# Kernel tuning notes

Hardware: AMD Instinct MI355X
Metric: run time of the kernel (lower is better)

## Reference

```python
import jax, jax.numpy as jnp
import numpy as np

EPS = 1e-8
K = 8  # group_size

def _l2norm(x):
    # matches torch F.normalize(p=2, eps): x / max(||x||, eps)
    n = jnp.linalg.norm(x, axis=-1, keepdims=True)
    return x / jnp.maximum(n, EPS)

def setup_inputs() -> dict:
    key = jax.random.key(0)
    k1, k2, k3, k4 = jax.random.split(key, 4)
    B, L, d = 8, 16384, 256
    max_groups = L // K
    token_vectors = jax.random.normal(k1, (B, L, d), dtype=jnp.float32)
    local_positions = jax.random.normal(k2, (K, d), dtype=jnp.float32)
    macro_positions = jax.random.normal(k3, (max_groups, d), dtype=jnp.float32)
    # learned params
    init_decay = 0.9
    decay_logit = jnp.full((d,), np.log(init_decay / (1.0 - init_decay)), dtype=jnp.float32)
    W_q = jax.random.normal(k4, (d, d), dtype=jnp.float32) * (1.0 / np.sqrt(d))
    return {"token_vectors": token_vectors, "local_positions": local_positions,
            "macro_positions": macro_positions, "decay_logit": decay_logit, "W_q": W_q}

def reference(token_vectors, local_positions, macro_positions, decay_logit, W_q):
    B, L, d = token_vectors.shape
    n_groups = L // K  # L chosen divisible by K; no remainder branch

    # ---- compute_groups: bind with local positions, mean over window, normalize
    full = token_vectors.reshape(B, n_groups, K, d)
    bound = full * local_positions[None, None]          # bind: elementwise product
    group_vecs = _l2norm(bound.mean(axis=2))            # [B, n_groups, d]

    # ---- causal EMA scan over groups with per-step L2 normalize
    alpha = jax.nn.sigmoid(decay_logit)                 # [d]
    def step(S, inp):
        g, mp = inp                                     # g: [B,d], mp: [d]
        S = _l2norm(alpha * S + (1.0 - alpha) * (g * mp))
        return S, S
    S0 = jnp.zeros((B, d), dtype=token_vectors.dtype)
    _, states = jax.lax.scan(step, S0, (group_vecs.transpose(1, 0, 2), macro_positions[:n_groups]))
    global_states = states.transpose(1, 0, 2)           # [B, n_groups, d]

    # ---- per-token queries from the state of the *previous* group
    t = jnp.arange(L)
    group_idx = t // K
    prev = jnp.maximum(group_idx - 1, 0)
    state = global_states[:, prev, :]                   # [B, L, d]
    state = jnp.where((group_idx < 1)[None, :, None], 0.0, state)
    local_pos = local_positions[t % K]                  # [L, d]
    queries = jnp.einsum('bld,ed->ble', state * local_pos[None], W_q)  # Linear: x @ W.T

    final_state = global_states[:, -1]
    return queries, final_state
```

## Files before the change

kernel.cpp:

```cpp
#include <hip/hip_runtime.h>
#include <hip/hip_bf16.h>

#define EPSV 1e-8f

typedef __attribute__((ext_vector_type(4))) float f32x4;
typedef __attribute__((ext_vector_type(8))) __bf16 bf16x8;
typedef __attribute__((ext_vector_type(8))) unsigned short ushort8;

static __device__ __forceinline__ unsigned short f2bf(float x) {
    __hip_bfloat16 h = __float2bfloat16(x);
    return *reinterpret_cast<unsigned short*>(&h);
}
static __device__ __forceinline__ float bf2f(unsigned short u) {
    __hip_bfloat16 h = *reinterpret_cast<__hip_bfloat16*>(&u);
    return __bfloat162float(h);
}

template <int CTRL, int RMASK = 0xf>
static __device__ __forceinline__ float dpp_add(float x) {
    int y = __builtin_amdgcn_update_dpp(0, __builtin_bit_cast(int, x), CTRL, RMASK, 0xf, true);
    return x + __builtin_bit_cast(float, y);
}

static __device__ __forceinline__ float wave_allsum(float x) {
    x = dpp_add<0xB1>(x);
    x = dpp_add<0x4E>(x);
    x = dpp_add<0x141>(x);
    x = dpp_add<0x140>(x);
    x = dpp_add<0x142, 0xa>(x);
    x = dpp_add<0x143, 0xc>(x);
    int t = __builtin_amdgcn_readlane(__builtin_bit_cast(int, x), 63);
    return __builtin_bit_cast(float, t);
}

__global__ __launch_bounds__(256) void build_bpt_kernel(const float* __restrict__ wq,
                                                        unsigned short* __restrict__ bpt) {
    int idx = blockIdx.x * 256 + threadIdx.x;
    int e = idx / 768;
    int j = idx - e * 768;
    int d = j & 255;
    int band = j >> 8;
    float w = wq[e * 256 + d];
    unsigned short hi = f2bf(w);
    unsigned short v;
    if (band == 1) v = f2bf(w - bf2f(hi));
    else           v = hi;
    bpt[idx] = v;
}

__global__ __launch_bounds__(256) void groupvec_kernel(const float* __restrict__ tv,
                                                       const float* __restrict__ lp,
                                                       const float* __restrict__ mp,
                                                       const float* __restrict__ dl,
                                                       float* __restrict__ v) {
    int bid = blockIdx.x;
    int g = bid & 2047;
    int d = threadIdx.x;
    const float* base = tv + (size_t)bid * 2048 + d;
    float acc = 0.f;
#pragma unroll
    for (int k = 0; k < 8; ++k)
        acc += base[k * 256] * lp[k * 256 + d];
    float m = acc * 0.125f;

    float p = m * m;
#pragma unroll
    for (int s = 1; s < 64; s <<= 1) p += __shfl_xor(p, s);
    __shared__ float red[4];
    if ((threadIdx.x & 63) == 0) red[threadIdx.x >> 6] = p;
    __syncthreads();
    float tot = red[0] + red[1] + red[2] + red[3];
    float n = sqrtf(tot);
    float inv = 1.0f / fmaxf(n, EPSV);

    float alpha = 1.0f / (1.0f + expf(-dl[d]));
    v[(size_t)bid * 256 + d] = (1.0f - alpha) * (m * inv) * mp[g * 256 + d];
}

__global__ __launch_bounds__(64) void scan_kernel(const float* __restrict__ v,
                                                  const float* __restrict__ dl,
                                                  float* __restrict__ states,
                                                  float* __restrict__ out) {
    int b = blockIdx.x;
    int lane = threadIdx.x;
    const float* vb = v + (size_t)b * 2048 * 256 + 4 * lane;
    float* sb = states + (size_t)b * 2048 * 256 + 4 * lane;

    f32x4 alpha;
#pragma unroll
    for (int i = 0; i < 4; ++i)
        alpha[i] = 1.0f / (1.0f + expf(-dl[4 * lane + i]));

    f32x4 buf[16];
#pragma unroll
    for (int j = 0; j < 16; ++j)
        buf[j] = *(const f32x4*)(vb + (size_t)j * 256);

    f32x4 w = {0.f, 0.f, 0.f, 0.f};
    float inv = 0.f;
    f32x4 S = {0.f, 0.f, 0.f, 0.f};

    for (int t = 0; t < 2048; t += 16) {
#pragma unroll
        for (int j = 0; j < 16; ++j) {
            const int g = t + j;
            f32x4 vcur = buf[j];
            const int gp = g + 16;
            if (gp < 2048) buf[j] = *(const f32x4*)(vb + (size_t)gp * 256);

            f32x4 u;
#pragma unroll
            for (int i = 0; i < 4; ++i) u[i] = fmaf(inv, w[i], vcur[i]);

            float m01 = fmaf(u[1], u[1], u[0] * u[0]);
            float m23 = fmaf(u[3], u[3], u[2] * u[2]);
            float ss = wave_allsum(m01 + m23);

            float ssc = fmaxf(ss, 1e-16f);
            float y0 = __builtin_amdgcn_rsqf(ssc);
            float h = 0.5f * ssc;
            float nr = fmaf(-h * y0, y0, 1.5f);
            inv = y0 * nr;

#pragma unroll
            for (int i = 0; i < 4; ++i) w[i] = alpha[i] * u[i];
#pragma unroll
            for (int i = 0; i < 4; ++i) S[i] = u[i] * inv;
            *(f32x4*)(sb + (size_t)g * 256) = S;
        }
    }
    *(f32x4*)(out + 33554432 + b * 256 + 4 * lane) = S;
}

__global__ __launch_bounds__(512) void queries_gemm_kernel(const float* __restrict__ states,
                                                           const float* __restrict__ lp,
                                                           const unsigned short* __restrict__ bpt,
                                                           float* __restrict__ out) {
    __shared__ unsigned short As[128 * 40];
    __shared__ unsigned short Bs[256 * 40];

    int tid = threadIdx.x;
    int lane = tid & 63;
    int wid = tid >> 6;
    int wm = wid >> 2;
    int wn = wid & 3;
    int row0 = blockIdx.x * 128;

    f32x4 acc[4][4];
#pragma unroll
    for (int i = 0; i < 4; ++i)
#pragma unroll
        for (int j = 0; j < 4; ++j) acc[i][j] = (f32x4){0.f, 0.f, 0.f, 0.f};

    int ar = tid >> 2;
    int aj0 = (tid & 3) * 8;
    int R = row0 + ar;
    int ab = R >> 14;
    int al = R & 16383;
    int ag = al >> 3;
    int ak = al & 7;
    const float* srow = (ag > 0) ? (states + ((size_t)(ab * 2048 + ag - 1)) * 256) : nullptr;
    const float* lrow = lp + ak * 256;

    int be = tid >> 1;
    int bj0 = (tid & 1) * 16;

    for (int c = 0; c < 24; ++c) {
        int kc = c * 32;
        int band = c >> 3;
        int dc = (c & 7) * 32;

        {
            float vals[8];
            if (ag == 0) {
#pragma unroll
                for (int i = 0; i < 8; ++i) vals[i] = 0.f;
            } else {
                f32x4 s0 = *(const f32x4*)(srow + dc + aj0);
                f32x4 s1 = *(const f32x4*)(srow + dc + aj0 + 4);
                f32x4 l0 = *(const f32x4*)(lrow + dc + aj0);
                f32x4 l1 = *(const f32x4*)(lrow + dc + aj0 + 4);
#pragma unroll
                for (int i = 0; i < 4; ++i) { vals[i] = s0[i] * l0[i]; vals[4 + i] = s1[i] * l1[i]; }
            }
            ushort8 h;
#pragma unroll
            for (int i = 0; i < 8; ++i) {
                unsigned short hi = f2bf(vals[i]);
                h[i] = (band < 2) ? hi : f2bf(vals[i] - bf2f(hi));
            }
            *(ushort8*)&As[ar * 40 + aj0] = h;
        }
        {
            const unsigned short* src = bpt + (size_t)be * 768 + kc + bj0;
            ushort8 b0 = *(const ushort8*)src;
            ushort8 b1 = *(const ushort8*)(src + 8);
            *(ushort8*)&Bs[be * 40 + bj0] = b0;
            *(ushort8*)&Bs[be * 40 + bj0 + 8] = b1;
        }
        __syncthreads();

        int lr = lane & 15;
        int lk = (lane >> 4) * 8;
        bf16x8 af[4], bfr[4];
#pragma unroll
        for (int mi = 0; mi < 4; ++mi) {
            ushort8 r = *(const ushort8*)&As[(wm * 64 + mi * 16 + lr) * 40 + lk];
            af[mi] = __builtin_bit_cast(bf16x8, r);
        }
#pragma unroll
        for (int ni = 0; ni < 4; ++ni) {
            ushort8 r = *(const ushort8*)&Bs[(wn * 64 + ni * 16 + lr) * 40 + lk];
            bfr[ni] = __builtin_bit_cast(bf16x8, r);
        }
#pragma unroll
        for (int mi = 0; mi < 4; ++mi)
#pragma unroll
            for (int ni = 0; ni < 4; ++ni)
                acc[mi][ni] = __builtin_amdgcn_mfma_f32_16x16x32_bf16(af[mi], bfr[ni], acc[mi][ni], 0, 0, 0);
        __syncthreads();
    }

    int cr = (lane >> 4) * 4;
    int cc = lane & 15;
#pragma unroll
    for (int mi = 0; mi < 4; ++mi) {
#pragma unroll
        for (int ni = 0; ni < 4; ++ni) {
            int Rg = row0 + wm * 64 + mi * 16 + cr;
            int E = wn * 64 + ni * 16 + cc;
#pragma unroll
            for (int q = 0; q < 4; ++q)
                out[(size_t)(Rg + q) * 256 + E] = acc[mi][ni][q];
        }
    }
}

extern "C" void kernel_launch(void* const* d_in, const int* in_sizes, int n_in,
                              void* d_out, int out_size, void* d_ws, size_t ws_size,
                              hipStream_t stream) {
    const float* tv = (const float*)d_in[0];
    const float* lp = (const float*)d_in[1];
    const float* mp = (const float*)d_in[2];
    const float* dl = (const float*)d_in[3];
    const float* wq = (const float*)d_in[4];
    float* out = (float*)d_out;

    float* v = (float*)d_ws;
    float* states = v + 4194304;
    unsigned short* bpt = (unsigned short*)(states + 4194304);

    build_bpt_kernel<<<768, 256, 0, stream>>>(wq, bpt);
    groupvec_kernel<<<16384, 256, 0, stream>>>(tv, lp, mp, dl, v);
    scan_kernel<<<8, 64, 0, stream>>>(v, dl, states, out);
    queries_gemm_kernel<<<1024, 512, 0, stream>>>(states, lp, bpt, out);
}
```

Measured before the change: 556.4 us.

## Break scan norm dependency and fold local positions into a per-group GEMM

The scan no longer waits on the norm of the current state before normalizing. It predicts the next squared norm algebraically from precomputed ||v||^2, the ||alpha*u||^2 term and the dot with the next input, so both wave reductions come off the critical recurrence. The local-position multiply moves into an expanded weight matrix (8x256 output columns per group), and the GEMM now works on per-group rows with precomputed bf16 hi/lo splits from a new convert kernel. This cuts A-side work in the GEMM. The cost is an extra kernel, a larger B matrix, and possible numerical drift from the expanded-norm formula.

Result: slower. 662.4 us (+19.1%).

```diff
diff --git a/kernel.cpp b/kernel.cpp
--- a/kernel.cpp
+++ b/kernel.cpp
@@ -4,6 +4,7 @@
 #define EPSV 1e-8f
 
 typedef __attribute__((ext_vector_type(4))) float f32x4;
+typedef __attribute__((ext_vector_type(4))) unsigned short u16x4;
 typedef __attribute__((ext_vector_type(8))) __bf16 bf16x8;
 typedef __attribute__((ext_vector_type(8))) unsigned short ushort8;
 
@@ -33,14 +34,17 @@
     return __builtin_bit_cast(float, t);
 }
 
-__global__ __launch_bounds__(256) void build_bpt_kernel(const float* __restrict__ wq,
+__global__ __launch_bounds__(256) void build_bpt_kernel(const float* __restrict__ lp,
+                                                        const float* __restrict__ wq,
                                                         unsigned short* __restrict__ bpt) {
     int idx = blockIdx.x * 256 + threadIdx.x;
-    int e = idx / 768;
-    int j = idx - e * 768;
+    int n = idx / 768;
+    int j = idx - n * 768;
     int d = j & 255;
     int band = j >> 8;
-    float w = wq[e * 256 + d];
+    int k = n >> 8;
+    int e = n & 255;
+    float w = lp[k * 256 + d] * wq[e * 256 + d];
     unsigned short hi = f2bf(w);
     unsigned short v;
     if (band == 1) v = f2bf(w - bf2f(hi));
@@ -52,7 +56,8 @@
                                                        const float* __restrict__ lp,
                                                        const float* __restrict__ mp,
                                                        const float* __restrict__ dl,
-                                                       float* __restrict__ v) {
+                                                       float* __restrict__ v,
+                                                       float* __restrict__ vv) {
     int bid = blockIdx.x;
     int g = bid & 2047;
     int d = threadIdx.x;
@@ -74,10 +79,20 @@
     float inv = 1.0f / fmaxf(n, EPSV);
 
     float alpha = 1.0f / (1.0f + expf(-dl[d]));
-    v[(size_t)bid * 256 + d] = (1.0f - alpha) * (m * inv) * mp[g * 256 + d];
+    float val = (1.0f - alpha) * (m * inv) * mp[g * 256 + d];
+    v[(size_t)bid * 256 + d] = val;
+
+    float q = val * val;
+#pragma unroll
+    for (int s = 1; s < 64; s <<= 1) q += __shfl_xor(q, s);
+    __shared__ float red2[4];
+    if ((threadIdx.x & 63) == 0) red2[threadIdx.x >> 6] = q;
+    __syncthreads();
+    if (threadIdx.x == 0) vv[bid] = red2[0] + red2[1] + red2[2] + red2[3];
 }
 
 __global__ __launch_bounds__(64) void scan_kernel(const float* __restrict__ v,
+                                                  const float* __restrict__ vv,
                                                   const float* __restrict__ dl,
                                                   float* __restrict__ states,
                                                   float* __restrict__ out) {
@@ -85,6 +100,7 @@
     int lane = threadIdx.x;
     const float* vb = v + (size_t)b * 2048 * 256 + 4 * lane;
     float* sb = states + (size_t)b * 2048 * 256 + 4 * lane;
+    const float* vvb = vv + b * 2048;
 
     f32x4 alpha;
 #pragma unroll
@@ -96,44 +112,89 @@
     for (int j = 0; j < 16; ++j)
         buf[j] = *(const f32x4*)(vb + (size_t)j * 256);
 
-    f32x4 w = {0.f, 0.f, 0.f, 0.f};
+    float vvreg = (lane < 16) ? vvb[lane] : 0.f;
+
+    f32x4 u = {0.f, 0.f, 0.f, 0.f};
+    f32x4 au = {0.f, 0.f, 0.f, 0.f};
+    f32x4 S = {0.f, 0.f, 0.f, 0.f};
     float inv = 0.f;
-    f32x4 S = {0.f, 0.f, 0.f, 0.f};
+    float ss = vvb[0];
 
     for (int t = 0; t < 2048; t += 16) {
+        float vvnext = 0.f;
+        if (t + 16 < 2048 && lane < 16) vvnext = vvb[t + 16 + lane];
 #pragma unroll
         for (int j = 0; j < 16; ++j) {
             const int g = t + j;
             f32x4 vcur = buf[j];
-            const int gp = g + 16;
-            if (gp < 2048) buf[j] = *(const f32x4*)(vb + (size_t)gp * 256);
-
-            f32x4 u;
-#pragma unroll
-            for (int i = 0; i < 4; ++i) u[i] = fmaf(inv, w[i], vcur[i]);
-
-            float m01 = fmaf(u[1], u[1], u[0] * u[0]);
-            float m23 = fmaf(u[3], u[3], u[2] * u[2]);
-            float ss = wave_allsum(m01 + m23);
+            if (g + 16 < 2048) buf[j] = *(const f32x4*)(vb + (size_t)(g + 16) * 256);
 
             float ssc = fmaxf(ss, 1e-16f);
-            float y0 = __builtin_amdgcn_rsqf(ssc);
-            float h = 0.5f * ssc;
-            float nr = fmaf(-h * y0, y0, 1.5f);
-            inv = y0 * nr;
-
-#pragma unroll
-            for (int i = 0; i < 4; ++i) w[i] = alpha[i] * u[i];
-#pragma unroll
-            for (int i = 0; i < 4; ++i) S[i] = u[i] * inv;
+            float invn = __builtin_amdgcn_rsqf(ssc);
+            float isq = __builtin_amdgcn_rcpf(ssc);
+
+            f32x4 un;
+#pragma unroll
+            for (int i = 0; i < 4; ++i) un[i] = fmaf(inv, au[i], vcur[i]);
+            u = un;
+#pragma unroll
+            for (int i = 0; i < 4; ++i) au[i] = alpha[i] * u[i];
+#pragma unroll
+            for (int i = 0; i < 4; ++i) S[i] = u[i] * invn;
             *(f32x4*)(sb + (size_t)g * 256) = S;
-        }
+
+            f32x4 vnx = buf[(j + 1) & 15];
+            float pp0 = fmaf(au[1], au[1], au[0] * au[0]);
+            float pp1 = fmaf(au[3], au[3], au[2] * au[2]);
+            float pv0 = fmaf(au[1], vnx[1], au[0] * vnx[0]);
+            float pv1 = fmaf(au[3], vnx[3], au[2] * vnx[2]);
+            float PP = wave_allsum(pp0 + pp1);
+            float PV = wave_allsum(pv0 + pv1);
+
+            float VVn;
+            if (j < 15) {
+                int ti = __builtin_amdgcn_readlane(__builtin_bit_cast(int, vvreg), j + 1);
+                VVn = __builtin_bit_cast(float, ti);
+            } else {
+                int ti = __builtin_amdgcn_readlane(__builtin_bit_cast(int, vvnext), 0);
+                VVn = __builtin_bit_cast(float, ti);
+            }
+
+            float inv2 = invn + invn;
+            ss = fmaf(PP, isq, fmaf(PV, inv2, VVn));
+            inv = invn;
+        }
+        vvreg = vvnext;
     }
     *(f32x4*)(out + 33554432 + b * 256 + 4 * lane) = S;
 }
 
-__global__ __launch_bounds__(512) void queries_gemm_kernel(const float* __restrict__ states,
-                                                           const float* __restrict__ lp,
+__global__ __launch_bounds__(256) void convert_kernel(const float* __restrict__ states,
+                                                      unsigned short* __restrict__ a_hi,
+                                                      unsigned short* __restrict__ a_lo) {
+    int idx = blockIdx.x * 256 + threadIdx.x;
+    int r = idx >> 6;
+    int d0 = (idx & 63) * 4;
+    int g = r & 2047;
+    u16x4 hi4, lo4;
+    if (g == 0) {
+        hi4 = (u16x4){0, 0, 0, 0};
+        lo4 = (u16x4){0, 0, 0, 0};
+    } else {
+        f32x4 s = *(const f32x4*)(states + (size_t)(r - 1) * 256 + d0);
+#pragma unroll
+        for (int i = 0; i < 4; ++i) {
+            unsigned short h = f2bf(s[i]);
+            hi4[i] = h;
+            lo4[i] = f2bf(s[i] - bf2f(h));
+        }
+    }
+    *(u16x4*)(a_hi + (size_t)r * 256 + d0) = hi4;
+    *(u16x4*)(a_lo + (size_t)r * 256 + d0) = lo4;
+}
+
+__global__ __launch_bounds__(512) void queries_gemm_kernel(const unsigned short* __restrict__ a_hi,
+                                                           const unsigned short* __restrict__ a_lo,
                                                            const unsigned short* __restrict__ bpt,
                                                            float* __restrict__ out) {
     __shared__ unsigned short As[128 * 40];
@@ -144,7 +205,8 @@
     int wid = tid >> 6;
     int wm = wid >> 2;
     int wn = wid & 3;
-    int row0 = blockIdx.x * 128;
+    int row0 = (blockIdx.x >> 3) * 128;
+    int col0 = (blockIdx.x & 7) * 256;
 
     f32x4 acc[4][4];
 #pragma unroll
@@ -154,16 +216,11 @@
 
     int ar = tid >> 2;
     int aj0 = (tid & 3) * 8;
-    int R = row0 + ar;
-    int ab = R >> 14;
-    int al = R & 16383;
-    int ag = al >> 3;
-    int ak = al & 7;
-    const float* srow = (ag > 0) ? (states + ((size_t)(ab * 2048 + ag - 1)) * 256) : nullptr;
-    const float* lrow = lp + ak * 256;
-
     int be = tid >> 1;
     int bj0 = (tid & 1) * 16;
+
+    const size_t arow_off = (size_t)(row0 + ar) * 256;
+    const size_t brow_off = (size_t)(col0 + be) * 768;
 
     for (int c = 0; c < 24; ++c) {
         int kc = c * 32;
@@ -171,28 +228,12 @@
         int dc = (c & 7) * 32;
 
         {
-            float vals[8];
-            if (ag == 0) {
-#pragma unroll
-                for (int i = 0; i < 8; ++i) vals[i] = 0.f;
-            } else {
-                f32x4 s0 = *(const f32x4*)(srow + dc + aj0);
-                f32x4 s1 = *(const f32x4*)(srow + dc + aj0 + 4);
-                f32x4 l0 = *(const f32x4*)(lrow + dc + aj0);
-                f32x4 l1 = *(const f32x4*)(lrow + dc + aj0 + 4);
-#pragma unroll
-                for (int i = 0; i < 4; ++i) { vals[i] = s0[i] * l0[i]; vals[4 + i] = s1[i] * l1[i]; }
-            }
-            ushort8 h;
-#pragma unroll
-            for (int i = 0; i < 8; ++i) {
-                unsigned short hi = f2bf(vals[i]);
-                h[i] = (band < 2) ? hi : f2bf(vals[i] - bf2f(hi));
-            }
+            const unsigned short* Ab = (band < 2) ? a_hi : a_lo;
+            ushort8 h = *(const ushort8*)(Ab + arow_off + dc + aj0);
             *(ushort8*)&As[ar * 40 + aj0] = h;
         }
         {
-            const unsigned short* src = bpt + (size_t)be * 768 + kc + bj0;
+            const unsigned short* src = bpt + brow_off + kc + bj0;
             ushort8 b0 = *(const ushort8*)src;
             ushort8 b1 = *(const ushort8*)(src + 8);
             *(ushort8*)&Bs[be * 40 + bj0] = b0;
@@ -228,10 +269,10 @@
 #pragma unroll
         for (int ni = 0; ni < 4; ++ni) {
             int Rg = row0 + wm * 64 + mi * 16 + cr;
-            int E = wn * 64 + ni * 16 + cc;
+            int E = col0 + wn * 64 + ni * 16 + cc;
 #pragma unroll
             for (int q = 0; q < 4; ++q)
-                out[(size_t)(Rg + q) * 256 + E] = acc[mi][ni][q];
+                out[(size_t)(Rg + q) * 2048 + E] = acc[mi][ni][q];
         }
     }
 }
@@ -249,9 +290,13 @@
     float* v = (float*)d_ws;
     float* states = v + 4194304;
     unsigned short* bpt = (unsigned short*)(states + 4194304);
-
-    build_bpt_kernel<<<768, 256, 0, stream>>>(wq, bpt);
-    groupvec_kernel<<<16384, 256, 0, stream>>>(tv, lp, mp, dl, v);
-    scan_kernel<<<8, 64, 0, stream>>>(v, dl, states, out);
-    queries_gemm_kernel<<<1024, 512, 0, stream>>>(states, lp, bpt, out);
-}
+    float* vv = (float*)(bpt + 1572864);
+    unsigned short* a_hi = (unsigned short*)v;
+    unsigned short* a_lo = a_hi + 4194304;
+
+    build_bpt_kernel<<<6144, 256, 0, stream>>>(lp, wq, bpt);
+    groupvec_kernel<<<16384, 256, 0, stream>>>(tv, lp, mp, dl, v, vv);
+    scan_kernel<<<8, 64, 0, stream>>>(v, vv, dl, states, out);
+    convert_kernel<<<4096, 256, 0, stream>>>(states, a_hi, a_lo);
+    queries_gemm_kernel<<<1024, 512, 0, stream>>>(a_hi, a_lo, bpt, out);
+}
```
